# Kernel optimization log

Hardware: AMD Instinct MI355X
Metric: run time of the kernel (lower is better)

## Reference

```python
import jax, jax.numpy as jnp
import numpy as np

W_BITS = 4  # active precision (max of supported_bits)
EPS = 0.005  # clamp margin from the original module


def _dequant_kbit(qweight, lut, w_bits):
    """Bit-plane LUT dequant.
    qweight: [w_bits, O, I//32] int32, plane b holds bit b (MSB-first code) of each
    weight's k-bit index, 32 consecutive input positions per int32 word (LSB-first
    within a word). lut: [O, 2**w_bits]. Returns dense weight [O, I].
    """
    O = qweight.shape[1]
    shifts = jnp.arange(32, dtype=jnp.int32)                     # bit position within word
    bits = (qweight[:, :, :, None] >> shifts) & 1                # [w_bits, O, I//32, 32]
    plane_w = (1 << (w_bits - 1 - jnp.arange(w_bits, dtype=jnp.int32)))
    idx = (bits * plane_w[:, None, None, None]).sum(axis=0)      # [O, I//32, 32]
    idx = idx.reshape(O, -1)                                     # [O, I]
    return jnp.take_along_axis(lut, idx, axis=1)                 # [O, I]


def _csr_dense(rows, cols, vals, O, I):
    """Scatter CSR (indptr=rows) into a dense [O, I] matrix."""
    nnz = cols.shape[0]
    k = jnp.arange(nnz, dtype=rows.dtype)
    row_ids = jnp.searchsorted(rows, k, side='right') - 1        # CSR row of each nnz
    return jnp.zeros((O, I), dtype=vals.dtype).at[row_ids, cols].add(vals)


def setup_inputs() -> dict:
    key = jax.random.key(0)
    ks = jax.random.split(key, 7)
    B, S, I, O = 4, 2048, 4096, 4096
    NNZ = 65536
    x = jax.random.normal(ks[0], (B, S, I), dtype=jnp.float32)
    qweight = jax.random.randint(ks[1], (W_BITS, O, I // 32), 0, 2147483647, dtype=jnp.int32)
    lut = jax.random.normal(ks[2], (O, 2 ** W_BITS), dtype=jnp.float32) * 0.05
    rows = jnp.sort(jax.random.randint(ks[3], (O + 1,), 0, NNZ, dtype=jnp.int32))
    rows = rows.at[0].set(0).at[-1].set(NNZ)                     # valid CSR indptr
    cols = jax.random.randint(ks[4], (NNZ,), 0, I, dtype=jnp.int32)
    vals = jax.random.normal(ks[5], (NNZ,), dtype=jnp.float32) * 0.01
    bias = jax.random.normal(ks[6], (O,), dtype=jnp.float32) * 0.01
    return {"x": x, "qweight": qweight, "lut": lut, "rows": rows,
            "cols": cols, "vals": vals, "bias": bias}


def reference(x, qweight, lut, rows, cols, vals, bias):
    O = qweight.shape[1]
    I = x.shape[-1]
    weight = _dequant_kbit(qweight, lut, W_BITS)                 # [O, I]
    y = jnp.einsum('bsi,oi->bso', x, weight)                     # dense quantized GEMM
    w_sp = _csr_dense(rows, cols, vals, O, I)                    # sparse outlier weights
    y = y + jnp.einsum('bsi,oi->bso', x, w_sp)
    y = y + bias
    fmax = jnp.finfo(x.dtype).max * (1.0 - EPS)
    return jnp.clip(y, -fmax, fmax)
```

## Files before the change

kernel.cpp:

```cpp
#include <hip/hip_runtime.h>
#include <stdint.h>

#define Mdim 8192
#define Ndim 4096
#define Kdim 4096

#define BM 256
#define BN 256
#define BK 32
#define NT (Kdim / BK)

typedef float f32x4 __attribute__((ext_vector_type(4)));
typedef __bf16 bf16x8 __attribute__((ext_vector_type(8)));
typedef unsigned short ushort_t;

#define FMAXC 3.3858093490333422e+38f

__device__ __forceinline__ ushort_t f2bf(float f) {
    unsigned u = __float_as_uint(f);
    u += 0x7fffu + ((u >> 16) & 1u);
    return (ushort_t)(u >> 16);
}

__device__ __forceinline__ void gload_lds16(const void* g, void* l) {
    __builtin_amdgcn_global_load_lds(
        (const __attribute__((address_space(1))) uint32_t*)g,
        (__attribute__((address_space(3))) uint32_t*)(uint32_t)(uintptr_t)l,
        16, 0, 0);
}

__global__ __launch_bounds__(128) void dequant_kernel(
        const int* __restrict__ qw, const float* __restrict__ lut,
        const int* __restrict__ rows, const int* __restrict__ cols,
        const float* __restrict__ vals, ushort_t* __restrict__ w16) {
    __shared__ float wrow[128 * 33];
    __shared__ float slut[16];
    const int o = blockIdx.x;
    const int t = threadIdx.x;

    if (t < 16) slut[t] = lut[o * 16 + t];
    __syncthreads();

    const int q0 = qw[0 * Ndim * 128 + o * 128 + t];
    const int q1 = qw[1 * Ndim * 128 + o * 128 + t];
    const int q2 = qw[2 * Ndim * 128 + o * 128 + t];
    const int q3 = qw[3 * Ndim * 128 + o * 128 + t];
    float* dst = &wrow[t * 33];
#pragma unroll
    for (int j = 0; j < 32; ++j) {
        int idx = (((q0 >> j) & 1) << 3) | (((q1 >> j) & 1) << 2) |
                  (((q2 >> j) & 1) << 1) | ((q3 >> j) & 1);
        dst[j] = slut[idx];
    }
    __syncthreads();

    const int beg = rows[o], end = rows[o + 1];
    for (int k = beg + t; k < end; k += 128) {
        int c = cols[k];
        atomicAdd(&wrow[c + (c >> 5)], vals[k]);
    }
    __syncthreads();

    __align__(16) ushort_t tmp[32];
#pragma unroll
    for (int j = 0; j < 32; ++j) tmp[j] = f2bf(dst[j]);
    uint4* dstg = (uint4*)(w16 + (size_t)o * Kdim + t * 32);
    const uint4* srcg = (const uint4*)tmp;
#pragma unroll
    for (int j = 0; j < 4; ++j) dstg[j] = srcg[j];
}

__global__ __launch_bounds__(256) void convx_kernel(
        const float* __restrict__ x, ushort_t* __restrict__ y) {
    size_t i = ((size_t)blockIdx.x * 256 + threadIdx.x) * 8;
    float4 a = *(const float4*)(x + i);
    float4 b = *(const float4*)(x + i + 4);
    __align__(16) ushort_t r[8] = {f2bf(a.x), f2bf(a.y), f2bf(a.z), f2bf(a.w),
                                   f2bf(b.x), f2bf(b.y), f2bf(b.z), f2bf(b.w)};
    *(uint4*)(y + i) = *(const uint4*)r;
}

__global__ __launch_bounds__(512, 2) void gemm_kernel(
        const ushort_t* __restrict__ A, const ushort_t* __restrict__ Bw,
        const float* __restrict__ bias, float* __restrict__ C) {
    __shared__ __align__(16) char lds[131072];

    const int wgid = blockIdx.x;
    const int swz = (wgid & 7) * 64 + (wgid >> 3);
    const int bn = swz & 15, bm = swz >> 4;
    const int m0 = bm * BM, n0 = bn * BN;

    const int tid = threadIdx.x;
    const int lane = tid & 63, wid = tid >> 6;
    const int wr = wid >> 2, wc = wid & 3;
    const int fr = lane & 15, kg = lane >> 4;

    const int sline = tid >> 3;
    const int slot = (tid & 7) ^ (sline & 7);
    const int srow0 = (sline << 1) + (slot >> 2);
    const int skel = (slot & 3) * 8;
    const ushort_t* gA = A + (size_t)(m0 + srow0) * Kdim + skel;
    const ushort_t* gB = Bw + (size_t)(n0 + srow0) * Kdim + skel;

    const int offL = (fr >> 1) * 128 + (((((fr & 1) << 2) | kg) ^ (fr >> 1)) << 4);

    f32x4 acc[8][4];
#pragma unroll
    for (int i = 0; i < 8; ++i)
#pragma unroll
        for (int j = 0; j < 4; ++j) acc[i][j] = (f32x4){0.f, 0.f, 0.f, 0.f};

    const ushort_t* pA = gA;
    const ushort_t* pB = gB;

    auto stageA = [&](int bufd) {
        char* d = lds + bufd * 16384 + tid * 16;
        gload_lds16(pA, d);
        gload_lds16(pA + (size_t)128 * Kdim, d + 8192);
    };
    auto stageB = [&](int bufd) {
        char* d = lds + 65536 + bufd * 16384 + tid * 16;
        gload_lds16(pB, d);
        gload_lds16(pB + (size_t)128 * Kdim, d + 8192);
    };

    stageA(0); stageB(0); pA += BK; pB += BK;
    stageA(1); stageB(1); pA += BK; pB += BK;
    asm volatile("s_waitcnt vmcnt(4)" ::: "memory");
    asm volatile("s_barrier" ::: "memory");

#pragma unroll 1
    for (int t = 0; t < NT; ++t) {
        const int bufi = t & 3;
        const int buf2 = (t + 2) & 3;
        const char* Ab = lds + bufi * 16384;
        const char* Bb = lds + 65536 + bufi * 16384;

        if (t + 2 < NT) {
            stageA(buf2);
            stageB(buf2);
        }
        pA += BK; pB += BK;

        bf16x8 Af[8], Bf[4];
#pragma unroll
        for (int n = 0; n < 4; ++n) {
            Af[n] = *(const bf16x8*)(Ab + wr * 8192 + n * 1024 + offL);
            Bf[n] = *(const bf16x8*)(Bb + wc * 4096 + n * 1024 + offL);
        }
#pragma unroll
        for (int m = 4; m < 8; ++m)
            Af[m] = *(const bf16x8*)(Ab + wr * 8192 + m * 1024 + offL);

        __builtin_amdgcn_s_setprio(1);
#pragma unroll
        for (int m = 0; m < 4; ++m)
#pragma unroll
            for (int n = 0; n < 4; ++n)
                acc[m][n] = __builtin_amdgcn_mfma_f32_16x16x32_bf16(
                    Af[m], Bf[n], acc[m][n], 0, 0, 0);
#pragma unroll
        for (int m = 4; m < 8; ++m)
#pragma unroll
            for (int n = 0; n < 4; ++n)
                acc[m][n] = __builtin_amdgcn_mfma_f32_16x16x32_bf16(
                    Af[m], Bf[n], acc[m][n], 0, 0, 0);
        __builtin_amdgcn_s_setprio(0);

        if (t < NT - 2) {
            asm volatile("s_waitcnt vmcnt(4)" ::: "memory");
        } else if (t == NT - 2) {
            asm volatile("s_waitcnt vmcnt(0)" ::: "memory");
        }
        asm volatile("s_barrier" ::: "memory");
    }

    const int rg = lane >> 4;
#pragma unroll
    for (int nf = 0; nf < 4; ++nf) {
        const int col = n0 + wc * 64 + nf * 16 + fr;
        const float bv = bias[col];
#pragma unroll
        for (int mf = 0; mf < 8; ++mf) {
            const int row = m0 + wr * 128 + mf * 16 + rg * 4;
            float* outp = C + (size_t)row * Ndim + col;
#pragma unroll
            for (int j = 0; j < 4; ++j) {
                float v = acc[mf][nf][j] + bv;
                v = fminf(fmaxf(v, -FMAXC), FMAXC);
                outp[(size_t)j * Ndim] = v;
            }
        }
    }
}

extern "C" void kernel_launch(void* const* d_in, const int* in_sizes, int n_in,
                              void* d_out, int out_size, void* d_ws, size_t ws_size,
                              hipStream_t stream) {
    const float* x    = (const float*)d_in[0];
    const int*   qw   = (const int*)d_in[1];
    const float* lut  = (const float*)d_in[2];
    const int*   rows = (const int*)d_in[3];
    const int*   cols = (const int*)d_in[4];
    const float* vals = (const float*)d_in[5];
    const float* bias = (const float*)d_in[6];
    float* out = (float*)d_out;

    ushort_t* x16 = (ushort_t*)d_ws;
    ushort_t* w16 = x16 + (size_t)Mdim * Kdim;

    hipLaunchKernelGGL(dequant_kernel, dim3(Ndim), dim3(128), 0, stream,
                       qw, lut, rows, cols, vals, w16);
    hipLaunchKernelGGL(convx_kernel, dim3((Mdim * Kdim) / (256 * 8)), dim3(256), 0, stream,
                       x, x16);
    hipLaunchKernelGGL(gemm_kernel, dim3((Mdim / BM) * (Ndim / BN)), dim3(512), 0, stream,
                       x16, w16, bias, out);
}
```

Baseline: 292.4 us.

## Double-buffer LDS fragment reads in registers and deepen global prefetch to three stages

```diff
diff --git a/kernel.cpp b/kernel.cpp
--- a/kernel.cpp
+++ b/kernel.cpp
@@ -123,53 +123,59 @@
         gload_lds16(pB, d);
         gload_lds16(pB + (size_t)128 * Kdim, d + 8192);
     };
+    auto readFrags = [&](bf16x8 (&FA)[8], bf16x8 (&FB)[4], int bufidx) {
+        const char* Ab = lds + bufidx * 16384;
+        const char* Bb = lds + 65536 + bufidx * 16384;
+#pragma unroll
+        for (int n = 0; n < 4; ++n) {
+            FA[n] = *(const bf16x8*)(Ab + wr * 8192 + n * 1024 + offL);
+            FB[n] = *(const bf16x8*)(Bb + wc * 4096 + n * 1024 + offL);
+        }
+#pragma unroll
+        for (int m = 4; m < 8; ++m)
+            FA[m] = *(const bf16x8*)(Ab + wr * 8192 + m * 1024 + offL);
+    };
+    auto mfmaTile = [&](bf16x8 (&FA)[8], bf16x8 (&FB)[4]) {
+        __builtin_amdgcn_s_setprio(1);
+#pragma unroll
+        for (int m = 0; m < 8; ++m)
+#pragma unroll
+            for (int n = 0; n < 4; ++n)
+                acc[m][n] = __builtin_amdgcn_mfma_f32_16x16x32_bf16(
+                    FA[m], FB[n], acc[m][n], 0, 0, 0);
+        __builtin_amdgcn_s_setprio(0);
+    };
 
     stageA(0); stageB(0); pA += BK; pB += BK;
     stageA(1); stageB(1); pA += BK; pB += BK;
+    stageA(2); stageB(2); pA += BK; pB += BK;
     asm volatile("s_waitcnt vmcnt(4)" ::: "memory");
     asm volatile("s_barrier" ::: "memory");
 
+    bf16x8 FAa[8], FAb[8];
+    bf16x8 FBa[4], FBb[4];
+    readFrags(FAa, FBa, 0);
+
 #pragma unroll 1
-    for (int t = 0; t < NT; ++t) {
-        const int bufi = t & 3;
-        const int buf2 = (t + 2) & 3;
-        const char* Ab = lds + bufi * 16384;
-        const char* Bb = lds + 65536 + bufi * 16384;
-
-        if (t + 2 < NT) {
-            stageA(buf2);
-            stageB(buf2);
-        }
+    for (int t = 0; t < NT; t += 2) {
+        readFrags(FAb, FBb, (t + 1) & 3);
+        if (t + 3 < NT) { stageA((t + 3) & 3); stageB((t + 3) & 3); }
         pA += BK; pB += BK;
-
-        bf16x8 Af[8], Bf[4];
-#pragma unroll
-        for (int n = 0; n < 4; ++n) {
-            Af[n] = *(const bf16x8*)(Ab + wr * 8192 + n * 1024 + offL);
-            Bf[n] = *(const bf16x8*)(Bb + wc * 4096 + n * 1024 + offL);
-        }
-#pragma unroll
-        for (int m = 4; m < 8; ++m)
-            Af[m] = *(const bf16x8*)(Ab + wr * 8192 + m * 1024 + offL);
-
-        __builtin_amdgcn_s_setprio(1);
-#pragma unroll
-        for (int m = 0; m < 4; ++m)
-#pragma unroll
-            for (int n = 0; n < 4; ++n)
-                acc[m][n] = __builtin_amdgcn_mfma_f32_16x16x32_bf16(
-                    Af[m], Bf[n], acc[m][n], 0, 0, 0);
-#pragma unroll
-        for (int m = 4; m < 8; ++m)
-#pragma unroll
-            for (int n = 0; n < 4; ++n)
-                acc[m][n] = __builtin_amdgcn_mfma_f32_16x16x32_bf16(
-                    Af[m], Bf[n], acc[m][n], 0, 0, 0);
-        __builtin_amdgcn_s_setprio(0);
-
-        if (t < NT - 2) {
+        mfmaTile(FAa, FBa);
+        if (t < NT - 3) {
             asm volatile("s_waitcnt vmcnt(4)" ::: "memory");
-        } else if (t == NT - 2) {
+        } else {
+            asm volatile("s_waitcnt vmcnt(0)" ::: "memory");
+        }
+        asm volatile("s_barrier" ::: "memory");
+
+        if (t + 2 < NT) readFrags(FAa, FBa, (t + 2) & 3);
+        if (t + 4 < NT) { stageA((t + 4) & 3); stageB((t + 4) & 3); }
+        pA += BK; pB += BK;
+        mfmaTile(FAb, FBb);
+        if (t + 1 < NT - 3) {
+            asm volatile("s_waitcnt vmcnt(4)" ::: "memory");
+        } else {
             asm volatile("s_waitcnt vmcnt(0)" ::: "memory");
         }
         asm volatile("s_barrier" ::: "memory");
```

Measured after the change: 290.3 us. No clear change (-0.7%).

## Split GEMM main loop into two half-phases interleaving LDS reads, loads, and MFMAs

Applied to the files above, without the earlier changes.

```diff
diff --git a/kernel.cpp b/kernel.cpp
--- a/kernel.cpp
+++ b/kernel.cpp
@@ -126,53 +126,96 @@
 
     stageA(0); stageB(0); pA += BK; pB += BK;
     stageA(1); stageB(1); pA += BK; pB += BK;
-    asm volatile("s_waitcnt vmcnt(4)" ::: "memory");
-    asm volatile("s_barrier" ::: "memory");
+    asm volatile("s_waitcnt vmcnt(4)");
+    __builtin_amdgcn_sched_barrier(0);
+    __builtin_amdgcn_s_barrier();
 
 #pragma unroll 1
-    for (int t = 0; t < NT; ++t) {
+    for (int t = 0; t < NT - 2; ++t) {
         const int bufi = t & 3;
         const int buf2 = (t + 2) & 3;
         const char* Ab = lds + bufi * 16384;
         const char* Bb = lds + 65536 + bufi * 16384;
 
-        if (t + 2 < NT) {
-            stageA(buf2);
-            stageB(buf2);
-        }
+        bf16x8 Af0[4], Bf[4];
+#pragma unroll
+        for (int m = 0; m < 4; ++m)
+            Af0[m] = *(const bf16x8*)(Ab + wr * 8192 + m * 1024 + offL);
+#pragma unroll
+        for (int n = 0; n < 4; ++n)
+            Bf[n] = *(const bf16x8*)(Bb + wc * 4096 + n * 1024 + offL);
+        stageA(buf2);
+        __builtin_amdgcn_s_barrier();
+        __builtin_amdgcn_s_setprio(1);
+#pragma unroll
+        for (int m = 0; m < 4; ++m)
+#pragma unroll
+            for (int n = 0; n < 4; ++n)
+                acc[m][n] = __builtin_amdgcn_mfma_f32_16x16x32_bf16(
+                    Af0[m], Bf[n], acc[m][n], 0, 0, 0);
+        __builtin_amdgcn_s_setprio(0);
+        __builtin_amdgcn_s_barrier();
+
+        bf16x8 Af1[4];
+#pragma unroll
+        for (int m = 0; m < 4; ++m)
+            Af1[m] = *(const bf16x8*)(Ab + wr * 8192 + (m + 4) * 1024 + offL);
+        stageB(buf2);
         pA += BK; pB += BK;
-
-        bf16x8 Af[8], Bf[4];
-#pragma unroll
-        for (int n = 0; n < 4; ++n) {
-            Af[n] = *(const bf16x8*)(Ab + wr * 8192 + n * 1024 + offL);
+        __builtin_amdgcn_s_barrier();
+        __builtin_amdgcn_s_setprio(1);
+#pragma unroll
+        for (int m = 0; m < 4; ++m)
+#pragma unroll
+            for (int n = 0; n < 4; ++n)
+                acc[m + 4][n] = __builtin_amdgcn_mfma_f32_16x16x32_bf16(
+                    Af1[m], Bf[n], acc[m + 4][n], 0, 0, 0);
+        __builtin_amdgcn_s_setprio(0);
+        asm volatile("s_waitcnt vmcnt(4)");
+        __builtin_amdgcn_sched_barrier(0);
+        __builtin_amdgcn_s_barrier();
+    }
+
+#pragma unroll 1
+    for (int t = NT - 2; t < NT; ++t) {
+        const int bufi = t & 3;
+        const char* Ab = lds + bufi * 16384;
+        const char* Bb = lds + 65536 + bufi * 16384;
+
+        bf16x8 Af0[4], Bf[4];
+#pragma unroll
+        for (int m = 0; m < 4; ++m)
+            Af0[m] = *(const bf16x8*)(Ab + wr * 8192 + m * 1024 + offL);
+#pragma unroll
+        for (int n = 0; n < 4; ++n)
             Bf[n] = *(const bf16x8*)(Bb + wc * 4096 + n * 1024 + offL);
-        }
-#pragma unroll
-        for (int m = 4; m < 8; ++m)
-            Af[m] = *(const bf16x8*)(Ab + wr * 8192 + m * 1024 + offL);
-
+        __builtin_amdgcn_s_barrier();
         __builtin_amdgcn_s_setprio(1);
 #pragma unroll
         for (int m = 0; m < 4; ++m)
 #pragma unroll
             for (int n = 0; n < 4; ++n)
                 acc[m][n] = __builtin_amdgcn_mfma_f32_16x16x32_bf16(
-                    Af[m], Bf[n], acc[m][n], 0, 0, 0);
-#pragma unroll
-        for (int m = 4; m < 8; ++m)
-#pragma unroll
-            for (int n = 0; n < 4; ++n)
-                acc[m][n] = __builtin_amdgcn_mfma_f32_16x16x32_bf16(
-                    Af[m], Bf[n], acc[m][n], 0, 0, 0);
-        __builtin_amdgcn_s_setprio(0);
-
-        if (t < NT - 2) {
-            asm volatile("s_waitcnt vmcnt(4)" ::: "memory");
-        } else if (t == NT - 2) {
-            asm volatile("s_waitcnt vmcnt(0)" ::: "memory");
-        }
-        asm volatile("s_barrier" ::: "memory");
+                    Af0[m], Bf[n], acc[m][n], 0, 0, 0);
+        __builtin_amdgcn_s_setprio(0);
+        __builtin_amdgcn_s_barrier();
+
+        bf16x8 Af1[4];
+#pragma unroll
+        for (int m = 0; m < 4; ++m)
+            Af1[m] = *(const bf16x8*)(Ab + wr * 8192 + (m + 4) * 1024 + offL);
+        __builtin_amdgcn_s_barrier();
+        __builtin_amdgcn_s_setprio(1);
+#pragma unroll
+        for (int m = 0; m < 4; ++m)
+#pragma unroll
+            for (int n = 0; n < 4; ++n)
+                acc[m + 4][n] = __builtin_amdgcn_mfma_f32_16x16x32_bf16(
+                    Af1[m], Bf[n], acc[m + 4][n], 0, 0, 0);
+        __builtin_amdgcn_s_setprio(0);
+        asm volatile("s_waitcnt vmcnt(0)");
+        __builtin_amdgcn_sched_barrier(0);
+        __builtin_amdgcn_s_barrier();
     }
 
     const int rg = lane >> 4;
```

Measured after the change: 291.4 us. About the same (-0.4%).

## Restructure GEMM main loop to BK=64 double buffering with scheduled interleave

Applied to the files above, without the earlier changes.

```diff
diff --git a/kernel.cpp b/kernel.cpp
--- a/kernel.cpp
+++ b/kernel.cpp
@@ -7,8 +7,8 @@
 
 #define BM 256
 #define BN 256
-#define BK 32
-#define NT (Kdim / BK)
+#define BK 64
+#define NT2 (Kdim / BK)
 
 typedef float f32x4 __attribute__((ext_vector_type(4)));
 typedef __bf16 bf16x8 __attribute__((ext_vector_type(8)));
@@ -28,6 +28,8 @@
         (__attribute__((address_space(3))) uint32_t*)(uint32_t)(uintptr_t)l,
         16, 0, 0);
 }
+
+#define SGB(mask, n) __builtin_amdgcn_sched_group_barrier(mask, n, 0)
 
 __global__ __launch_bounds__(128) void dequant_kernel(
         const int* __restrict__ qw, const float* __restrict__ lut,
@@ -95,14 +97,13 @@
     const int wr = wid >> 2, wc = wid & 3;
     const int fr = lane & 15, kg = lane >> 4;
 
-    const int sline = tid >> 3;
-    const int slot = (tid & 7) ^ (sline & 7);
-    const int srow0 = (sline << 1) + (slot >> 2);
-    const int skel = (slot & 3) * 8;
-    const ushort_t* gA = A + (size_t)(m0 + srow0) * Kdim + skel;
-    const ushort_t* gB = Bw + (size_t)(n0 + srow0) * Kdim + skel;
-
-    const int offL = (fr >> 1) * 128 + (((((fr & 1) << 2) | kg) ^ (fr >> 1)) << 4);
+    const int srow = tid >> 3;
+    const int scol = (((tid & 7) ^ (srow & 7)) * 8);
+    const ushort_t* gA = A + (size_t)(m0 + srow) * Kdim + scol;
+    const ushort_t* gB = Bw + (size_t)(n0 + srow) * Kdim + scol;
+
+    const int off0 = fr * 128 + (((kg) ^ (fr & 7)) << 4);
+    const int off1 = fr * 128 + (((4 | kg) ^ (fr & 7)) << 4);
 
     f32x4 acc[8][4];
 #pragma unroll
@@ -110,69 +111,76 @@
 #pragma unroll
         for (int j = 0; j < 4; ++j) acc[i][j] = (f32x4){0.f, 0.f, 0.f, 0.f};
 
-    const ushort_t* pA = gA;
-    const ushort_t* pB = gB;
-
-    auto stageA = [&](int bufd) {
-        char* d = lds + bufd * 16384 + tid * 16;
-        gload_lds16(pA, d);
-        gload_lds16(pA + (size_t)128 * Kdim, d + 8192);
-    };
-    auto stageB = [&](int bufd) {
-        char* d = lds + 65536 + bufd * 16384 + tid * 16;
-        gload_lds16(pB, d);
-        gload_lds16(pB + (size_t)128 * Kdim, d + 8192);
-    };
-
-    stageA(0); stageB(0); pA += BK; pB += BK;
-    stageA(1); stageB(1); pA += BK; pB += BK;
-    asm volatile("s_waitcnt vmcnt(4)" ::: "memory");
-    asm volatile("s_barrier" ::: "memory");
-
-#pragma unroll 1
-    for (int t = 0; t < NT; ++t) {
-        const int bufi = t & 3;
-        const int buf2 = (t + 2) & 3;
-        const char* Ab = lds + bufi * 16384;
-        const char* Bb = lds + 65536 + bufi * 16384;
-
-        if (t + 2 < NT) {
-            stageA(buf2);
-            stageB(buf2);
+    auto stage = [&](int buf, int t1) {
+        const ushort_t* sa = gA + (size_t)t1 * BK;
+        const ushort_t* sb = gB + (size_t)t1 * BK;
+        char* da = lds + buf * 65536 + tid * 16;
+        char* db = da + 32768;
+#pragma unroll
+        for (int j = 0; j < 4; ++j) {
+            gload_lds16(sa + (size_t)j * 64 * Kdim, da + j * 8192);
+            gload_lds16(sb + (size_t)j * 64 * Kdim, db + j * 8192);
         }
-        pA += BK; pB += BK;
-
-        bf16x8 Af[8], Bf[4];
-#pragma unroll
-        for (int n = 0; n < 4; ++n) {
-            Af[n] = *(const bf16x8*)(Ab + wr * 8192 + n * 1024 + offL);
-            Bf[n] = *(const bf16x8*)(Bb + wc * 4096 + n * 1024 + offL);
-        }
-#pragma unroll
-        for (int m = 4; m < 8; ++m)
-            Af[m] = *(const bf16x8*)(Ab + wr * 8192 + m * 1024 + offL);
-
-        __builtin_amdgcn_s_setprio(1);
-#pragma unroll
-        for (int m = 0; m < 4; ++m)
+    };
+    auto readA = [&](bf16x8 (&FA)[8], const char* Ab, int off) {
+#pragma unroll
+        for (int m = 0; m < 8; ++m)
+            FA[m] = *(const bf16x8*)(Ab + wr * 16384 + m * 2048 + off);
+    };
+    auto readB = [&](bf16x8 (&FB)[4], const char* Bb, int off) {
+#pragma unroll
+        for (int n = 0; n < 4; ++n)
+            FB[n] = *(const bf16x8*)(Bb + wc * 8192 + n * 2048 + off);
+    };
+    auto mfmaK = [&](bf16x8 (&FA)[8], bf16x8 (&FB)[4]) {
+#pragma unroll
+        for (int m = 0; m < 8; ++m)
 #pragma unroll
             for (int n = 0; n < 4; ++n)
                 acc[m][n] = __builtin_amdgcn_mfma_f32_16x16x32_bf16(
-                    Af[m], Bf[n], acc[m][n], 0, 0, 0);
-#pragma unroll
-        for (int m = 4; m < 8; ++m)
-#pragma unroll
-            for (int n = 0; n < 4; ++n)
-                acc[m][n] = __builtin_amdgcn_mfma_f32_16x16x32_bf16(
-                    Af[m], Bf[n], acc[m][n], 0, 0, 0);
+                    FA[m], FB[n], acc[m][n], 0, 0, 0);
+    };
+
+    stage(0, 0);
+    asm volatile("s_waitcnt vmcnt(0)");
+    __builtin_amdgcn_sched_barrier(0);
+    __builtin_amdgcn_s_barrier();
+
+#pragma unroll 1
+    for (int t = 0; t < NT2 - 1; ++t) {
+        const char* Ab = lds + (t & 1) * 65536;
+        const char* Bb = Ab + 32768;
+
+        bf16x8 A0[8], B0[4], A1[8], B1[4];
+        readA(A0, Ab, off0); readB(B0, Bb, off0);
+        stage((t + 1) & 1, t + 1);
+        readA(A1, Ab, off1); readB(B1, Bb, off1);
+
+        __builtin_amdgcn_s_setprio(1);
+        mfmaK(A0, B0);
+        mfmaK(A1, B1);
         __builtin_amdgcn_s_setprio(0);
 
-        if (t < NT - 2) {
-            asm volatile("s_waitcnt vmcnt(4)" ::: "memory");
-        } else if (t == NT - 2) {
-            asm volatile("s_waitcnt vmcnt(0)" ::: "memory");
-        }
-        asm volatile("s_barrier" ::: "memory");
+        SGB(0x100, 12);
+#pragma unroll
+        for (int i = 0; i < 4; ++i) { SGB(0x30, 2); SGB(0x8, 4); }
+#pragma unroll
+        for (int i = 0; i < 6; ++i) { SGB(0x100, 2); SGB(0x8, 2); }
+        SGB(0x8, 36);
+
+        asm volatile("s_waitcnt vmcnt(0)");
+        __builtin_amdgcn_sched_barrier(0);
+        __builtin_amdgcn_s_barrier();
+    }
+
+    {
+        const char* Ab = lds + ((NT2 - 1) & 1) * 65536;
+        const char* Bb = Ab + 32768;
+        bf16x8 A0[8], B0[4], A1[8], B1[4];
+        readA(A0, Ab, off0); readB(B0, Bb, off0);
+        readA(A1, Ab, off1); readB(B1, Bb, off1);
+        mfmaK(A0, B0);
+        mfmaK(A1, B1);
     }
 
     const int rg = lane >> 4;
```

After: 275.7 us. 1.06x faster.
